# Performance work log

Measured on AMD Instinct MI355X. Metric: run time of the kernel, lower is better.

The kernel has to match this reference:

```python
import jax, jax.numpy as jnp
import numpy as np

E = 8           # num_local_experts
H = 1024        # hidden_size
F = 1024        # moe_ffn_hidden_size (per-half; fc1 out = 2*F due to GLU)
T = 16384       # total dispatched tokens
GLU_LINEAR_OFFSET = 1.0


def setup_inputs() -> dict:
    key = jax.random.key(0)
    ks = jax.random.split(key, 7)
    s1 = 1.0 / np.sqrt(H)
    s2 = 1.0 / np.sqrt(F)
    return {
        "hidden_states": jax.random.normal(ks[0], (T, H), jnp.float32),
        "tokens_per_expert": jnp.full((E,), T // E, dtype=jnp.int64),
        "probs": jax.random.uniform(ks[1], (T,), jnp.float32),
        # expert params; torch Linear W is [out,in], stored here as [in,out] (same math)
        "W1": jax.random.uniform(ks[2], (E, H, 2 * F), jnp.float32, -s1, s1),
        "b1": jax.random.uniform(ks[3], (E, 2 * F), jnp.float32, -s1, s1),
        "W2": jax.random.uniform(ks[4], (E, F, H), jnp.float32, -s2, s2),
        "b2": jax.random.uniform(ks[5], (E, H), jnp.float32, -s2, s2),
    }


def reference(hidden_states, tokens_per_expert, probs, W1, b1, W2, b2):
    # Tokens arrive grouped contiguously by expert with equal counts (as in
    # setup_inputs), so the split/loop/cat in the torch module is exactly a
    # reshape + grouped (batched) GEMM over the expert axis.
    e = W1.shape[0]
    t, h = hidden_states.shape
    x = hidden_states.reshape(e, t // e, h)            # [E, Tpe, H]
    p = probs.reshape(e, t // e)                       # [E, Tpe]
    # fc1 (gated)
    y = jnp.einsum('eth,ehf->etf', x, W1) + b1[:, None, :]  # [E, Tpe, 2F]
    gate, lin = jnp.split(y, 2, axis=-1)
    a = jax.nn.silu(gate) * (lin + GLU_LINEAR_OFFSET)       # [E, Tpe, F]
    a = a * p[..., None]                                    # per-token scale
    # fc2
    out = jnp.einsum('etf,efh->eth', a, W2) + b2[:, None, :]
    return out.reshape(t, h)
```

## Files before the change

kernel.cpp:

```cpp
#include <hip/hip_runtime.h>
#include <hip/hip_bf16.h>
#include <stdint.h>

#define T_TOK 16384
#define H_DIM 1024
#define F_DIM 1024
#define E_NUM 8
#define TPE   2048

typedef unsigned short u16;
typedef __attribute__((ext_vector_type(8))) short bf16x8;
typedef __attribute__((ext_vector_type(4))) float f32x4;
typedef __attribute__((ext_vector_type(8))) u16 u16x8;

__device__ __forceinline__ u16 f2bf(float x) {
  unsigned int u = __float_as_uint(x);
  u = (u + 0x7fffu + ((u >> 16) & 1u)) >> 16;
  return (u16)u;
}

#define GLD16(gp, lp)                                                          \
  __builtin_amdgcn_global_load_lds(                                            \
      (const __attribute__((address_space(1))) void*)(gp),                     \
      (__attribute__((address_space(3))) void*)(lp), 16, 0, 0)

__global__ __launch_bounds__(256) void cvt_f32_bf16(
    const float* __restrict__ src, u16* __restrict__ dst, int n8) {
  int stride = gridDim.x * blockDim.x;
  for (int i = blockIdx.x * blockDim.x + threadIdx.x; i < n8; i += stride) {
    const float4* s = (const float4*)(src + (size_t)i * 8);
    float4 a = s[0], b = s[1];
    u16x8 o;
    o[0] = f2bf(a.x); o[1] = f2bf(a.y); o[2] = f2bf(a.z); o[3] = f2bf(a.w);
    o[4] = f2bf(b.x); o[5] = f2bf(b.y); o[6] = f2bf(b.z); o[7] = f2bf(b.w);
    *(u16x8*)(dst + (size_t)i * 8) = o;
  }
}

__global__ __launch_bounds__(256) void transpose_cvt(
    const float* __restrict__ src, u16* __restrict__ dst, int R, int C) {
  __shared__ float tile[64][65];
  int nCt = C >> 6, nRt = R >> 6;
  int per = nCt * nRt;
  int b = blockIdx.x;
  int e = b / per;
  int r2 = b - e * per;
  int rt = r2 / nCt, ct = r2 - rt * nCt;
  const float* s = src + (size_t)e * R * C + (size_t)(rt << 6) * C + (ct << 6);
  int t = threadIdx.x;
  int lr = t >> 4, lc = (t & 15) << 2;
#pragma unroll
  for (int i = 0; i < 4; i++) {
    float4 v = *(const float4*)(s + (size_t)(lr + i * 16) * C + lc);
    tile[lr + i * 16][lc + 0] = v.x;
    tile[lr + i * 16][lc + 1] = v.y;
    tile[lr + i * 16][lc + 2] = v.z;
    tile[lr + i * 16][lc + 3] = v.w;
  }
  __syncthreads();
  u16* d = dst + (size_t)e * C * R + (size_t)(ct << 6) * R + (rt << 6);
  int orow = t >> 2, ok = (t & 3) << 4;
  u16x8 o0, o1;
#pragma unroll
  for (int i = 0; i < 8; i++) o0[i] = f2bf(tile[ok + i][orow]);
#pragma unroll
  for (int i = 0; i < 8; i++) o1[i] = f2bf(tile[ok + 8 + i][orow]);
  *(u16x8*)(d + (size_t)orow * R + ok) = o0;
  *(u16x8*)(d + (size_t)orow * R + ok + 8) = o1;
}


#define DSA4(b, h, ks)                                                         \
  _Pragma("unroll") for (int m_ = 0; m_ < 4; ++m_)                             \
      aF[m_] = *(const bf16x8*)(sm + (b) * 32768 + aRowBase +                  \
                                ((h) * 4 + m_) * 2048 + koff[ks]);

#define DSB4(b, ks)                                                            \
  _Pragma("unroll") for (int n_ = 0; n_ < 4; ++n_)                             \
      bF[n_] = *(const bf16x8*)(sm + 65536 + (b) * 32768 + bRowBase +          \
                                n_ * 2048 + koff[ks]);

#define MFMAP(h)                                                               \
  _Pragma("unroll") for (int n_ = 0; n_ < 4; ++n_)                             \
  _Pragma("unroll") for (int m_ = 0; m_ < 4; ++m_)                             \
      acc[(h) * 4 + m_][n_] = __builtin_amdgcn_mfma_f32_16x16x32_bf16(         \
          aF[m_], bF[n_], acc[(h) * 4 + m_][n_], 0, 0, 0);

#define PF_A(db, q, d) GLD16(aP[q] + (d), sm + (db) * 32768 + (q) * 8192 + tid * 16)
#define PF_B(db, q, d) GLD16(bP[q] + (d), sm + 65536 + (db) * 32768 + (q) * 8192 + tid * 16)

#define VMW(N) asm volatile("s_waitcnt vmcnt(" #N ")" ::: "memory");

#define PHASEK(b, ks, h, PFC, WTC)                                             \
  do {                                                                         \
    DSA4(b, h, ks);                                                            \
    if ((h) == 0) { DSB4(b, ks); }                                             \
    PFC                                                                        \
    __builtin_amdgcn_s_barrier();                                              \
    asm volatile("s_waitcnt lgkmcnt(0)" ::: "memory");                         \
    __builtin_amdgcn_s_setprio(1);                                             \
    MFMAP(h);                                                                  \
    __builtin_amdgcn_s_setprio(0);                                             \
    WTC                                                                        \
    __builtin_amdgcn_s_barrier();                                              \
  } while (0)

#define KLOOP_BODY                                                             \
  PF_B(0, 0, 0); PF_B(0, 1, 0); PF_B(0, 2, 0); PF_B(0, 3, 0);                  \
  PF_A(0, 0, 0); PF_A(0, 1, 0); PF_A(0, 2, 0); PF_A(0, 3, 0);                  \
  PF_B(1, 0, 64); PF_B(1, 1, 64); PF_B(1, 2, 64); PF_B(1, 3, 64);              \
  VMW(4)                                                                       \
  __builtin_amdgcn_s_barrier();                                                \
  for (int it = 0; it < 7; ++it) {                                             \
    PHASEK(0, 0, 0, PF_A(1, 0, 64); PF_A(1, 1, 64);, );                        \
    PHASEK(0, 0, 1, PF_A(1, 2, 64); PF_A(1, 3, 64);, );                        \
    PHASEK(0, 1, 0, , );                                                       \
    PHASEK(0, 1, 1,                                                            \
           PF_B(0, 0, 128); PF_B(0, 1, 128); PF_B(0, 2, 128);                  \
           PF_B(0, 3, 128);, VMW(4));                                          \
    PHASEK(1, 0, 0, PF_A(0, 0, 128); PF_A(0, 1, 128);, );                      \
    PHASEK(1, 0, 1, PF_A(0, 2, 128); PF_A(0, 3, 128);, );                      \
    PHASEK(1, 1, 0, , );                                                       \
    PHASEK(1, 1, 1,                                                            \
           PF_B(1, 0, 192); PF_B(1, 1, 192); PF_B(1, 2, 192);                  \
           PF_B(1, 3, 192);, VMW(4));                                          \
    _Pragma("unroll") for (int q_ = 0; q_ < 4; ++q_) {                         \
      aP[q_] += 128; bP[q_] += 128;                                            \
    }                                                                          \
  }                                                                            \
                   \
  PHASEK(0, 0, 0, PF_A(1, 0, 64); PF_A(1, 1, 64);, );                          \
  PHASEK(0, 0, 1, PF_A(1, 2, 64); PF_A(1, 3, 64);, );                          \
  PHASEK(0, 1, 0, , );                                                         \
  PHASEK(0, 1, 1, , VMW(0));                                                   \
  PHASEK(1, 0, 0, , );                                                         \
  PHASEK(1, 0, 1, , );                                                         \
  PHASEK(1, 1, 0, , );                                                         \
  PHASEK(1, 1, 1, , );

__global__ __launch_bounds__(512, 2) void gemm1_8p(
    const u16* __restrict__ xbf, const u16* __restrict__ w1t,
    const float* __restrict__ b1, const float* __restrict__ probs,
    u16* __restrict__ abf) {
  extern __shared__ char sm[];
  const int tid = threadIdx.x;
  const int lane = tid & 63;
  const int wid = tid >> 6;
  const int wm = wid >> 2, wn = wid & 3;
  const int bid = blockIdx.x;
  const int e = bid & 7;
  const int inner = bid >> 3;
  const int mt = inner >> 3, ct = inner & 7;
  const int tokBase = e * TPE + mt * 256;
  const int c0 = ct * 128;
  const int lrow = lane & 15, lkhi = lane >> 4;

  const u16* aP[4]; const u16* bP[4];
#pragma unroll
  for (int q = 0; q < 4; ++q) {
    int lin = q * 8192 + tid * 16;
    int lg = lin ^ (((lin >> 7) & 7) << 4);
    int row = lg >> 7, kk = (lg & 127) >> 1;
    aP[q] = xbf + (size_t)(tokBase + row) * H_DIM + kk;
    int col = (((row >> 5) & 1) << 10) + c0 + ((row >> 6) << 5) + (row & 31);
    bP[q] = w1t + (size_t)(e * 2 * F_DIM + col) * H_DIM + kk;
  }
  const int aRowBase = (wm * 128 + lrow) * 128;
  const int bRowBase = (wn * 64 + lrow) * 128;
  int koff[2];
#pragma unroll
  for (int ks = 0; ks < 2; ++ks)
    koff[ks] = ((ks << 6) | (lkhi << 4)) ^ ((lane & 7) << 4);

  f32x4 acc[8][4];
#pragma unroll
  for (int i = 0; i < 8; ++i)
#pragma unroll
    for (int j = 0; j < 4; ++j) acc[i][j] = f32x4{0.f, 0.f, 0.f, 0.f};
  bf16x8 aF[4], bF[4];

  KLOOP_BODY

#pragma unroll
  for (int j = 0; j < 2; ++j) {
    int cf = c0 + wn * 32 + j * 16 + lrow;
    float gb = b1[e * 2 * F_DIM + cf];
    float lb = b1[e * 2 * F_DIM + F_DIM + cf];
#pragma unroll
    for (int i = 0; i < 8; ++i) {
      int trow = tokBase + wm * 128 + i * 16 + lkhi * 4;
#pragma unroll
      for (int r = 0; r < 4; ++r) {
        float g = acc[i][j][r] + gb;
        float l = acc[i][j + 2][r] + lb + 1.0f;
        float p = probs[trow + r];
        float sig = 1.0f / (1.0f + __expf(-g));
        abf[(size_t)(trow + r) * F_DIM + cf] = f2bf(g * sig * l * p);
      }
    }
  }
}

__global__ __launch_bounds__(512, 2) void gemm2_8p(
    const u16* __restrict__ abf, const u16* __restrict__ w2t,
    const float* __restrict__ b2, float* __restrict__ out) {
  extern __shared__ char sm[];
  const int tid = threadIdx.x;
  const int lane = tid & 63;
  const int wid = tid >> 6;
  const int wm = wid >> 2, wn = wid & 3;
  const int bid = blockIdx.x;
  const int e = bid & 7;
  const int inner = bid >> 3;
  const int mt = inner >> 2, nt = inner & 3;
  const int tokBase = e * TPE + mt * 256;
  const int h0 = nt * 256;
  const int lrow = lane & 15, lkhi = lane >> 4;

  const u16* aP[4]; const u16* bP[4];
#pragma unroll
  for (int q = 0; q < 4; ++q) {
    int lin = q * 8192 + tid * 16;
    int lg = lin ^ (((lin >> 7) & 7) << 4);
    int row = lg >> 7, kk = (lg & 127) >> 1;
    aP[q] = abf + (size_t)(tokBase + row) * F_DIM + kk;
    bP[q] = w2t + (size_t)(e * H_DIM + h0 + row) * F_DIM + kk;
  }
  const int aRowBase = (wm * 128 + lrow) * 128;
  const int bRowBase = (wn * 64 + lrow) * 128;
  int koff[2];
#pragma unroll
  for (int ks = 0; ks < 2; ++ks)
    koff[ks] = ((ks << 6) | (lkhi << 4)) ^ ((lane & 7) << 4);

  f32x4 acc[8][4];
#pragma unroll
  for (int i = 0; i < 8; ++i)
#pragma unroll
    for (int j = 0; j < 4; ++j) acc[i][j] = f32x4{0.f, 0.f, 0.f, 0.f};
  bf16x8 aF[4], bF[4];

  KLOOP_BODY

#pragma unroll
  for (int j = 0; j < 4; ++j) {
    int h = h0 + wn * 64 + j * 16 + lrow;
    float bb = b2[e * H_DIM + h];
#pragma unroll
    for (int i = 0; i < 8; ++i) {
      int trow = tokBase + wm * 128 + i * 16 + lkhi * 4;
#pragma unroll
      for (int r = 0; r < 4; ++r)
        out[(size_t)(trow + r) * H_DIM + h] = acc[i][j][r] + bb;
    }
  }
}

extern "C" void kernel_launch(void* const* d_in, const int* in_sizes, int n_in,
                              void* d_out, int out_size, void* d_ws,
                              size_t ws_size, hipStream_t stream) {
  const float* x     = (const float*)d_in[0];
  const float* probs = (const float*)d_in[2];
  const float* W1    = (const float*)d_in[3];
  const float* b1    = (const float*)d_in[4];
  const float* W2    = (const float*)d_in[5];
  const float* b2    = (const float*)d_in[6];
  float* out = (float*)d_out;

  if (ws_size < 117440512u) return;
  char* ws = (char*)d_ws;
  u16* xbf = (u16*)(ws);
  u16* w1t = (u16*)(ws + 33554432);
  u16* w2t = (u16*)(ws + 67108864);
  u16* abf = (u16*)(ws + 83886080);

  (void)hipFuncSetAttribute(reinterpret_cast<const void*>(gemm1_8p),
                            hipFuncAttributeMaxDynamicSharedMemorySize, 131072);
  (void)hipFuncSetAttribute(reinterpret_cast<const void*>(gemm2_8p),
                            hipFuncAttributeMaxDynamicSharedMemorySize, 131072);

  cvt_f32_bf16<<<2048, 256, 0, stream>>>(x, xbf, (T_TOK * H_DIM) / 8);
  transpose_cvt<<<E_NUM * (2 * F_DIM / 64) * (H_DIM / 64), 256, 0, stream>>>(
      W1, w1t, H_DIM, 2 * F_DIM);
  transpose_cvt<<<E_NUM * (H_DIM / 64) * (F_DIM / 64), 256, 0, stream>>>(
      W2, w2t, F_DIM, H_DIM);
  gemm1_8p<<<E_NUM * 8 * 8, 512, 131072, stream>>>(xbf, w1t, b1, probs, abf);
  gemm2_8p<<<E_NUM * 8 * 4, 512, 131072, stream>>>(abf, w2t, b2, out);
}
```

Before: 160.5 us.

## Replace 8-phase interleaved K-loop with simple double-buffered stage/compute schedule

Replaces the fine-grained 8-phase K-loop, which interleaved partial LDS fragment loads, global-to-LDS prefetches and MFMA groups with barriers between them, with a coarser schedule. Each step now issues a full stage prefetch, waits, and computes a whole 64-K buffer using all 8 A fragments at once. The change cuts the barrier count and simplifies the code. In exchange it loses prefetch/compute overlap, because the code waits on vmcnt right after issuing the next stage, and the larger fragment set raises register pressure under launch_bounds(512,2).

```diff
diff --git a/kernel.cpp b/kernel.cpp
--- a/kernel.cpp
+++ b/kernel.cpp
@@ -70,73 +70,60 @@
 }
 
 
-#define DSA4(b, h, ks)                                                         \
-  _Pragma("unroll") for (int m_ = 0; m_ < 4; ++m_)                             \
-      aF[m_] = *(const bf16x8*)(sm + (b) * 32768 + aRowBase +                  \
-                                ((h) * 4 + m_) * 2048 + koff[ks]);
-
-#define DSB4(b, ks)                                                            \
-  _Pragma("unroll") for (int n_ = 0; n_ < 4; ++n_)                             \
-      bF[n_] = *(const bf16x8*)(sm + 65536 + (b) * 32768 + bRowBase +          \
-                                n_ * 2048 + koff[ks]);
-
-#define MFMAP(h)                                                               \
-  _Pragma("unroll") for (int n_ = 0; n_ < 4; ++n_)                             \
-  _Pragma("unroll") for (int m_ = 0; m_ < 4; ++m_)                             \
-      acc[(h) * 4 + m_][n_] = __builtin_amdgcn_mfma_f32_16x16x32_bf16(         \
-          aF[m_], bF[n_], acc[(h) * 4 + m_][n_], 0, 0, 0);
+#define MFMA(a, b, c) __builtin_amdgcn_mfma_f32_16x16x32_bf16((a), (b), (c), 0, 0, 0)
 
 #define PF_A(db, q, d) GLD16(aP[q] + (d), sm + (db) * 32768 + (q) * 8192 + tid * 16)
 #define PF_B(db, q, d) GLD16(bP[q] + (d), sm + 65536 + (db) * 32768 + (q) * 8192 + tid * 16)
 
+#define STAGE(db, off)                                                         \
+  PF_B(db, 0, off); PF_B(db, 1, off); PF_B(db, 2, off); PF_B(db, 3, off);      \
+  PF_A(db, 0, off); PF_A(db, 1, off); PF_A(db, 2, off); PF_A(db, 3, off);
+
 #define VMW(N) asm volatile("s_waitcnt vmcnt(" #N ")" ::: "memory");
 
-#define PHASEK(b, ks, h, PFC, WTC)                                             \
-  do {                                                                         \
-    DSA4(b, h, ks);                                                            \
-    if ((h) == 0) { DSB4(b, ks); }                                             \
-    PFC                                                                        \
+#define COMPUTE(b)                                                             \
+  _Pragma("unroll") for (int ks_ = 0; ks_ < 2; ++ks_) {                        \
+    bf16x8 aF[8], bF[4];                                                       \
+    _Pragma("unroll") for (int m_ = 0; m_ < 8; ++m_)                           \
+        aF[m_] = *(const bf16x8*)(sm + (b) * 32768 + aRowBase + m_ * 2048 +    \
+                                  koff[ks_]);                                  \
+    _Pragma("unroll") for (int n_ = 0; n_ < 4; ++n_)                           \
+        bF[n_] = *(const bf16x8*)(sm + 65536 + (b) * 32768 + bRowBase +        \
+                                  n_ * 2048 + koff[ks_]);                      \
+    __builtin_amdgcn_s_setprio(1);                                             \
+    _Pragma("unroll") for (int n_ = 0; n_ < 4; ++n_)                           \
+    _Pragma("unroll") for (int m_ = 0; m_ < 8; ++m_)                           \
+        acc[m_][n_] = MFMA(aF[m_], bF[n_], acc[m_][n_]);                       \
+    __builtin_amdgcn_s_setprio(0);                                             \
+  }
+
+#define KLOOP_BODY                                                             \
+  STAGE(0, 0)                                              \
+  for (int it = 0; it < 7; ++it) {                                             \
+    __builtin_amdgcn_s_barrier();          \
+    STAGE(1, 64)                                       \
+    VMW(8)                                     \
+    __builtin_amdgcn_s_barrier();            \
+    COMPUTE(0)                                                   \
     __builtin_amdgcn_s_barrier();                                              \
-    asm volatile("s_waitcnt lgkmcnt(0)" ::: "memory");                         \
-    __builtin_amdgcn_s_setprio(1);                                             \
-    MFMAP(h);                                                                  \
-    __builtin_amdgcn_s_setprio(0);                                             \
-    WTC                                                                        \
+    STAGE(0, 128)                                      \
+    VMW(8)                                                                     \
     __builtin_amdgcn_s_barrier();                                              \
-  } while (0)
-
-#define KLOOP_BODY                                                             \
-  PF_B(0, 0, 0); PF_B(0, 1, 0); PF_B(0, 2, 0); PF_B(0, 3, 0);                  \
-  PF_A(0, 0, 0); PF_A(0, 1, 0); PF_A(0, 2, 0); PF_A(0, 3, 0);                  \
-  PF_B(1, 0, 64); PF_B(1, 1, 64); PF_B(1, 2, 64); PF_B(1, 3, 64);              \
-  VMW(4)                                                                       \
-  __builtin_amdgcn_s_barrier();                                                \
-  for (int it = 0; it < 7; ++it) {                                             \
-    PHASEK(0, 0, 0, PF_A(1, 0, 64); PF_A(1, 1, 64);, );                        \
-    PHASEK(0, 0, 1, PF_A(1, 2, 64); PF_A(1, 3, 64);, );                        \
-    PHASEK(0, 1, 0, , );                                                       \
-    PHASEK(0, 1, 1,                                                            \
-           PF_B(0, 0, 128); PF_B(0, 1, 128); PF_B(0, 2, 128);                  \
-           PF_B(0, 3, 128);, VMW(4));                                          \
-    PHASEK(1, 0, 0, PF_A(0, 0, 128); PF_A(0, 1, 128);, );                      \
-    PHASEK(1, 0, 1, PF_A(0, 2, 128); PF_A(0, 3, 128);, );                      \
-    PHASEK(1, 1, 0, , );                                                       \
-    PHASEK(1, 1, 1,                                                            \
-           PF_B(1, 0, 192); PF_B(1, 1, 192); PF_B(1, 2, 192);                  \
-           PF_B(1, 3, 192);, VMW(4));                                          \
+    COMPUTE(1)                                                 \
     _Pragma("unroll") for (int q_ = 0; q_ < 4; ++q_) {                         \
       aP[q_] += 128; bP[q_] += 128;                                            \
     }                                                                          \
   }                                                                            \
-                   \
-  PHASEK(0, 0, 0, PF_A(1, 0, 64); PF_A(1, 1, 64);, );                          \
-  PHASEK(0, 0, 1, PF_A(1, 2, 64); PF_A(1, 3, 64);, );                          \
-  PHASEK(0, 1, 0, , );                                                         \
-  PHASEK(0, 1, 1, , VMW(0));                                                   \
-  PHASEK(1, 0, 0, , );                                                         \
-  PHASEK(1, 0, 1, , );                                                         \
-  PHASEK(1, 1, 0, , );                                                         \
-  PHASEK(1, 1, 1, , );
+                             \
+  __builtin_amdgcn_s_barrier();                                                \
+  STAGE(1, 64)                                            \
+  VMW(8)                                                                       \
+  __builtin_amdgcn_s_barrier();                                                \
+  COMPUTE(0)                                                      \
+  __builtin_amdgcn_s_barrier();                                                \
+  VMW(0)                                                                       \
+  __builtin_amdgcn_s_barrier();                                                \
+  COMPUTE(1)
 
 __global__ __launch_bounds__(512, 2) void gemm1_8p(
     const u16* __restrict__ xbf, const u16* __restrict__ w1t,
@@ -177,7 +164,6 @@
   for (int i = 0; i < 8; ++i)
 #pragma unroll
     for (int j = 0; j < 4; ++j) acc[i][j] = f32x4{0.f, 0.f, 0.f, 0.f};
-  bf16x8 aF[4], bF[4];
 
   KLOOP_BODY
 
@@ -238,7 +224,6 @@
   for (int i = 0; i < 8; ++i)
 #pragma unroll
     for (int j = 0; j < 4; ++j) acc[i][j] = f32x4{0.f, 0.f, 0.f, 0.f};
-  bf16x8 aF[4], bF[4];
 
   KLOOP_BODY
 
```

New measurement: 162.4 us. About the same (+1.1%).
